# Performance work log

Hardware: AMD Instinct MI355X
Metric: run time of the kernel (lower is better)

Reference implementation:

```python
import jax, jax.numpy as jnp
import numpy as np

STATE = 256
IN = 128
OUT = 128


def setup_inputs() -> dict:
    key = jax.random.key(0)
    ks = jax.random.split(key, 10)
    u = jax.random.normal(ks[0], (8, 2048, IN), dtype=jnp.float32)
    x0_re = jax.random.normal(ks[1], (8, STATE), dtype=jnp.float32)
    x0_im = jax.random.normal(ks[2], (8, STATE), dtype=jnp.float32)
    # A init: 2*pi*rand angles on unit circle, scaled by 10 (enforce_stability=True)
    theta = 2.0 * jnp.pi * jax.random.uniform(ks[3], (STATE,), dtype=jnp.float32)
    A_re = 10.0 * jnp.cos(theta)
    A_im = 10.0 * jnp.sin(theta)
    # complex randn: real/imag parts each have variance 1/2
    inv_sqrt2 = 1.0 / np.sqrt(2.0)
    sB = inv_sqrt2 / np.sqrt(STATE + IN)
    B_re = jax.random.normal(ks[4], (IN, STATE), dtype=jnp.float32) * sB
    B_im = jax.random.normal(ks[5], (IN, STATE), dtype=jnp.float32) * sB
    sC = inv_sqrt2 / np.sqrt(STATE + OUT)
    C_re = jax.random.normal(ks[6], (STATE, OUT), dtype=jnp.float32) * sC
    C_im = jax.random.normal(ks[7], (STATE, OUT), dtype=jnp.float32) * sC
    D = jnp.zeros((IN, OUT), dtype=jnp.float32)
    b = jnp.zeros((OUT,), dtype=jnp.float32)
    return {"u": u, "x0_re": x0_re, "x0_im": x0_im, "A_re": A_re, "A_im": A_im,
            "B_re": B_re, "B_im": B_im, "C_re": C_re, "C_im": C_im, "D": D, "b": b}


def reference(u, x0_re, x0_im, A_re, A_im, B_re, B_im, C_re, C_im, D, b):
    cdt = jnp.complex64
    length = u.shape[1]
    A = (A_re + 1j * A_im).astype(cdt)
    # enforce_stability: map poles inside unit disc
    A = A / jnp.sqrt(A * jnp.conj(A) + 1.0)
    # Vandermonde powers A^t for t in [0, length]  -> [length+1, n]
    Aps = A[None, :] ** jnp.arange(length + 1)[:, None]
    Bm = (B_re + 1j * B_im).astype(cdt)
    uB = u.astype(cdt) @ Bm  # [batch, length, n]
    # FFT-based causal convolution of Aps[:-1] ([length, n]) with uB
    T = 2 ** int(np.ceil(np.log2(2 * length - 1)))
    AF = jnp.fft.fft(Aps[:-1], n=T, axis=0)      # [T, n]
    UF = jnp.fft.fft(uB, n=T, axis=1)            # [batch, T, n]
    x = jnp.fft.ifft(AF[None] * UF, axis=1)[:, :length]  # [batch, length, n]
    # add initial-state contribution A^t * x0
    x0 = (x0_re + 1j * x0_im).astype(cdt)
    x = x + Aps[1:][None] * x0[:, None, :]
    Cm = (C_re + 1j * C_im).astype(cdt)
    y = jnp.real(x @ Cm) + u @ D + b
    return y, x[:, -1]
```

## Files before the change

kernel.cpp:

```cpp
#include <hip/hip_runtime.h>
#include <math.h>

#define BATCH 8
#define T 2048
#define N 256
#define INF 128
#define OUTF 128
#define L 16
#define LOG2L 4
#define NC (T / L)
#define KTOT 640
#define NKS 20
#define NKU 4
#define UBS 516

typedef __attribute__((ext_vector_type(8))) short short8;
typedef __attribute__((ext_vector_type(4))) float f32x4;

__device__ __forceinline__ unsigned short f2b(float f) {
    union { float f; unsigned u; } x; x.f = f;
    unsigned r = (x.u + 0x7FFFu + ((x.u >> 16) & 1u)) >> 16;
    return (unsigned short)r;
}
__device__ __forceinline__ float b2f(unsigned short s) {
    union { unsigned u; float f; } x; x.u = ((unsigned)s) << 16;
    return x.f;
}

__global__ __launch_bounds__(256) void k_prep(const float* __restrict__ Are,
                                              const float* __restrict__ Aim,
                                              const float* __restrict__ Bre,
                                              const float* __restrict__ Bim,
                                              const float* __restrict__ Cre,
                                              const float* __restrict__ Cim,
                                              const float* __restrict__ D,
                                              float2* __restrict__ Apow,
                                              unsigned short* __restrict__ Bswz,
                                              unsigned short* __restrict__ Bswz2) {
    int blk = blockIdx.x;
    int tid = threadIdx.x;
    if (blk < 40) {
        int unit = blk * 4 + (tid >> 6);
        int ks = unit >> 3, ot = unit & 7;
        int l = tid & 63;
        int o = ot * 16 + (l & 15);
        int k0 = ks * 32 + (l >> 4) * 8;
        short8 out;
#pragma unroll
        for (int j = 0; j < 8; ++j) {
            int gk = k0 + j;
            float v = (gk < 256) ? Cre[gk * OUTF + o]
                    : (gk < 512) ? -Cim[(gk - 256) * OUTF + o]
                                 : D[(gk - 512) * OUTF + o];
            out[j] = (short)f2b(v);
        }
        *(short8*)(Bswz + ((size_t)unit * 64 + l) * 8) = out;
    } else if (blk < 72) {
        int unit = (blk - 40) * 4 + (tid >> 6);
        int l = tid & 63;
        int col = (unit & 31) * 16 + (l & 15);
        int k0 = (unit >> 5) * 32 + (l >> 4) * 8;
        short8 out;
#pragma unroll
        for (int j = 0; j < 8; ++j) {
            int gk = k0 + j;
            float v = (col < 256) ? Bre[gk * N + col] : Bim[gk * N + col - 256];
            out[j] = (short)f2b(v);
        }
        *(short8*)(Bswz2 + ((size_t)unit * 64 + l) * 8) = out;
    } else {
        int n = tid;
        float ar = Are[n], ai = Aim[n];
        float inv = 1.0f / sqrtf(ar * ar + ai * ai + 1.0f);
        ar *= inv; ai *= inv;
        float pr = ar, pi = ai;
        for (int j = 0; j < L; ++j) {
            Apow[j * N + n] = make_float2(pr, pi);
            float nr = pr * ar - pi * ai;
            float ni = pr * ai + pi * ar;
            pr = nr; pi = ni;
        }
    }
}

__global__ __launch_bounds__(512, 8) void kU_scan(const float* __restrict__ u,
                                                  const unsigned short* __restrict__ Bswz2,
                                                  const float2* __restrict__ Apow,
                                                  unsigned short* __restrict__ xbb,
                                                  float2* __restrict__ carr) {
    __shared__ float uB[16][UBS];
    int tid = threadIdx.x;
    int lane = tid & 63;
    int w = tid >> 6;
    size_t rowg0 = (size_t)blockIdx.x * 16;
    const float* uprow = u + (rowg0 + (lane & 15)) * INF + (lane >> 4) * 8;

    f32x4 acc[4];
#pragma unroll
    for (int i = 0; i < 4; ++i) acc[i] = (f32x4){0.f, 0.f, 0.f, 0.f};

    const short8* Bfr2 = (const short8*)Bswz2;
#pragma unroll
    for (int ks = 0; ks < NKU; ++ks) {
        float4 a0 = *(const float4*)(uprow + ks * 32);
        float4 a1 = *(const float4*)(uprow + ks * 32 + 4);
        short8 af;
        af[0] = (short)f2b(a0.x); af[1] = (short)f2b(a0.y);
        af[2] = (short)f2b(a0.z); af[3] = (short)f2b(a0.w);
        af[4] = (short)f2b(a1.x); af[5] = (short)f2b(a1.y);
        af[6] = (short)f2b(a1.z); af[7] = (short)f2b(a1.w);
#pragma unroll
        for (int i = 0; i < 4; ++i) {
            int ct = w * 4 + i;
            short8 bf = Bfr2[(size_t)(ks * 32 + ct) * 64 + lane];
            acc[i] = __builtin_amdgcn_mfma_f32_16x16x32_bf16(af, bf, acc[i], 0, 0, 0);
        }
    }
    {
        int rbase = (lane >> 4) * 4;
        int cb = lane & 15;
#pragma unroll
        for (int i = 0; i < 4; ++i) {
            int col = (w * 4 + i) * 16 + cb;
#pragma unroll
            for (int r = 0; r < 4; ++r)
                uB[rbase + r][col] = acc[i][r];
        }
    }
    __syncthreads();

    if (tid < 256) {
        int n = tid;
        int b = (int)(rowg0 >> 11);
        int c = (int)((rowg0 & 2047) >> LOG2L);
        float2 a = Apow[n];
        float xr = 0.f, xi = 0.f;
#pragma unroll
        for (int j = 0; j < 16; ++j) {
            float ur = uB[j][n];
            float ui = uB[j][256 + n];
            float nr = fmaf(a.x, xr, fmaf(-a.y, xi, ur));
            float ni = fmaf(a.x, xi, fmaf(a.y, xr, ui));
            xr = nr; xi = ni;
            size_t rowg = rowg0 + j;
            xbb[rowg * 512 + n]       = f2b(xr);
            xbb[rowg * 512 + 256 + n] = f2b(xi);
        }
        carr[((size_t)b * NC + c) * N + n] = make_float2(xr, xi);
    }
}

__global__ __launch_bounds__(256) void k2_carry(const float* __restrict__ x0re,
                                                const float* __restrict__ x0im,
                                                const float2* __restrict__ Apow,
                                                float2* __restrict__ carr,
                                                float* __restrict__ out_tail,
                                                int tail_mode) {
    int b = blockIdx.x, n = threadIdx.x;
    float pr = x0re[b * N + n], pi = x0im[b * N + n];
    float2 aL = Apow[(L - 1) * N + n];
#pragma unroll 8
    for (int c = 0; c < NC; ++c) {
        size_t off = ((size_t)b * NC + c) * N + n;
        float2 f = carr[off];
        carr[off] = make_float2(pr, pi);
        float nr = f.x + aL.x * pr - aL.y * pi;
        float ni = f.y + aL.x * pi + aL.y * pr;
        pr = nr; pi = ni;
    }
    if (tail_mode == 2) {
        out_tail[(b * N + n) * 2 + 0] = pr;
        out_tail[(b * N + n) * 2 + 1] = pi;
    } else if (tail_mode == 1) {
        out_tail[b * N + n] = pr;
    }
}

__global__ __launch_bounds__(256) void k3_mfma(const unsigned short* __restrict__ xbb,
                                               const float2* __restrict__ Apow,
                                               const float2* __restrict__ carr,
                                               const float* __restrict__ u,
                                               const unsigned short* __restrict__ Bswz,
                                               const float* __restrict__ bias,
                                               float* __restrict__ y) {
    __shared__ short8 Bs[2][1024];
    int tid = threadIdx.x;
    int lane = tid & 63;
    int w = tid >> 6;
    size_t rowg = (size_t)blockIdx.x * 64 + w * 16 + (lane & 15);
    int koff = (lane >> 4) * 8;
    int t = (int)(rowg & 2047);
    int b = (int)(rowg >> 11);
    int j = t & (L - 1);
    int c = t >> LOG2L;
    const float4* Ap4 = (const float4*)(Apow + (size_t)j * N);
    const float4* Cv4 = (const float4*)(carr + ((size_t)b * NC + c) * N);
    const unsigned short* arow = xbb + rowg * 512 + koff;
    const float* urow = u + rowg * INF + koff;
    const char* Bbytes = (const char*)Bswz;

    f32x4 acc[8];
#pragma unroll
    for (int ot = 0; ot < 8; ++ot) acc[ot] = (f32x4){0.f, 0.f, 0.f, 0.f};

    auto KApair = [](int p, int& ka, int& kb) {
        if (p < 8) { ka = p; kb = p + 8; }
        else if (p == 8) { ka = 16; kb = 17; }
        else { ka = 18; kb = 19; }
    };

    auto STAGEB = [&](int p, int buf) {
        int ka, kb; KApair(p, ka, kb);
#pragma unroll
        for (int i = 0; i < 4; ++i) {
            int seg = w * 4 + i;
            int k = (seg < 8) ? ka : kb;
            const char* src = Bbytes + (size_t)k * 8192 + (size_t)(seg & 7) * 1024 + (size_t)lane * 16;
            __builtin_amdgcn_global_load_lds(
                (const __attribute__((address_space(1))) unsigned int*)src,
                (__attribute__((address_space(3))) unsigned int*)((char*)&Bs[buf][0] + seg * 1024),
                16, 0, 0);
        }
    };

    STAGEB(0, 0);
    __syncthreads();

    int cur = 0;
    for (int p = 0; p < 10; ++p) {
        if (p < 9) STAGEB(p + 1, cur ^ 1);

        short8 afa, afb;
        if (p < 8) {
            short8 xre = *(const short8*)(arow + p * 32);
            short8 xim = *(const short8*)(arow + (p + 8) * 32);
            int n0 = p * 32 + koff;
            float4 ap[4], vv[4];
#pragma unroll
            for (int q = 0; q < 4; ++q) {
                ap[q] = Ap4[(n0 >> 1) + q];
                vv[q] = Cv4[(n0 >> 1) + q];
            }
#pragma unroll
            for (int e = 0; e < 8; ++e) {
                float4 aq = ap[e >> 1];
                float4 vq = vv[e >> 1];
                float pr = (e & 1) ? aq.z : aq.x;
                float pi = (e & 1) ? aq.w : aq.y;
                float vr = (e & 1) ? vq.z : vq.x;
                float vi = (e & 1) ? vq.w : vq.y;
                afa[e] = (short)f2b(b2f((unsigned short)xre[e]) + (pr * vr - pi * vi));
                afb[e] = (short)f2b(b2f((unsigned short)xim[e]) + (pr * vi + pi * vr));
            }
        } else {
            int ks2a = (p == 8) ? 0 : 2;
            float4 a0 = *(const float4*)(urow + ks2a * 32);
            float4 a1 = *(const float4*)(urow + ks2a * 32 + 4);
            afa[0] = (short)f2b(a0.x); afa[1] = (short)f2b(a0.y);
            afa[2] = (short)f2b(a0.z); afa[3] = (short)f2b(a0.w);
            afa[4] = (short)f2b(a1.x); afa[5] = (short)f2b(a1.y);
            afa[6] = (short)f2b(a1.z); afa[7] = (short)f2b(a1.w);
            float4 b0 = *(const float4*)(urow + (ks2a + 1) * 32);
            float4 b1 = *(const float4*)(urow + (ks2a + 1) * 32 + 4);
            afb[0] = (short)f2b(b0.x); afb[1] = (short)f2b(b0.y);
            afb[2] = (short)f2b(b0.z); afb[3] = (short)f2b(b0.w);
            afb[4] = (short)f2b(b1.x); afb[5] = (short)f2b(b1.y);
            afb[6] = (short)f2b(b1.z); afb[7] = (short)f2b(b1.w);
        }

#pragma unroll
        for (int ot = 0; ot < 8; ++ot) {
            short8 bf = Bs[cur][ot * 64 + lane];
            acc[ot] = __builtin_amdgcn_mfma_f32_16x16x32_bf16(afa, bf, acc[ot], 0, 0, 0);
        }
#pragma unroll
        for (int ot = 0; ot < 8; ++ot) {
            short8 bf = Bs[cur][512 + ot * 64 + lane];
            acc[ot] = __builtin_amdgcn_mfma_f32_16x16x32_bf16(afb, bf, acc[ot], 0, 0, 0);
        }

        __syncthreads();
        cur ^= 1;
    }

    int colb = lane & 15;
    int rq = lane >> 4;
    size_t rowout = (size_t)blockIdx.x * 64 + w * 16 + rq * 4;
#pragma unroll
    for (int ot = 0; ot < 8; ++ot) {
        int o = ot * 16 + colb;
        float bv = bias[o];
#pragma unroll
        for (int r = 0; r < 4; ++r) {
            y[(rowout + r) * OUTF + o] = acc[ot][r] + bv;
        }
    }
}

extern "C" void kernel_launch(void* const* d_in, const int* in_sizes, int n_in,
                              void* d_out, int out_size, void* d_ws, size_t ws_size,
                              hipStream_t stream) {
    const float* u    = (const float*)d_in[0];
    const float* x0re = (const float*)d_in[1];
    const float* x0im = (const float*)d_in[2];
    const float* Are  = (const float*)d_in[3];
    const float* Aim  = (const float*)d_in[4];
    const float* Bre  = (const float*)d_in[5];
    const float* Bim  = (const float*)d_in[6];
    const float* Cre  = (const float*)d_in[7];
    const float* Cim  = (const float*)d_in[8];
    const float* D    = (const float*)d_in[9];
    const float* bias = (const float*)d_in[10];
    float* y = (float*)d_out;

    char* ws = (char*)d_ws;
    float2* Apow = (float2*)ws;
    char* p = ws + (size_t)L * N * sizeof(float2);
    float2* carr = (float2*)p;
    p += (size_t)BATCH * NC * N * sizeof(float2);
    unsigned short* xbb = (unsigned short*)p;
    p += (size_t)BATCH * T * 512 * sizeof(unsigned short);
    unsigned short* Bswz = (unsigned short*)p;
    p += (size_t)NKS * 8 * 64 * 8 * sizeof(unsigned short);
    unsigned short* Bswz2 = (unsigned short*)p;

    const int ysz = BATCH * T * OUTF;
    const int tail_elems = out_size - ysz;
    int tail_mode = (tail_elems >= BATCH * N * 2) ? 2
                  : (tail_elems >= BATCH * N) ? 1 : 0;
    float* tail = y + ysz;

    k_prep<<<73, 256, 0, stream>>>(Are, Aim, Bre, Bim, Cre, Cim, D, Apow, Bswz, Bswz2);
    kU_scan<<<BATCH * NC, 512, 0, stream>>>(u, Bswz2, Apow, xbb, carr);
    k2_carry<<<BATCH, 256, 0, stream>>>(x0re, x0im, Apow, carr, tail, tail_mode);
    k3_mfma<<<(BATCH * T) / 64, 256, 0, stream>>>(xbb, Apow, carr, u, Bswz, bias, y);
}
```

Before: 55.12 us.

## Stage scan output through LDS for vectorized stores and prefetch A operands

In the chunk-scan kernel, per-step scattered 2-byte bf16 stores of the state are replaced by writing the fp32 state back into the shared uB tile, then a cooperative pass packs rows into 16-byte bf16 vector stores. In the output GEMM kernel, the x/Apow/Cv and u fragment loads for the next k-step are issued before the current MFMAs, a software prefetch that hides global load latency. This costs an extra barrier and LDS round trip, and more live registers.

Result: no change. 54.49 us (median of 3 runs) (-1.1%).

```diff
diff --git a/kernel.cpp b/kernel.cpp
--- a/kernel.cpp
+++ b/kernel.cpp
@@ -142,11 +142,29 @@
             float nr = fmaf(a.x, xr, fmaf(-a.y, xi, ur));
             float ni = fmaf(a.x, xi, fmaf(a.y, xr, ui));
             xr = nr; xi = ni;
-            size_t rowg = rowg0 + j;
-            xbb[rowg * 512 + n]       = f2b(xr);
-            xbb[rowg * 512 + 256 + n] = f2b(xi);
+            uB[j][n] = xr;
+            uB[j][256 + n] = xi;
         }
         carr[((size_t)b * NC + c) * N + n] = make_float2(xr, xi);
+    }
+    __syncthreads();
+
+    {
+        int row = tid & 15;
+        int cg  = tid >> 4;
+#pragma unroll
+        for (int half = 0; half < 2; ++half) {
+            int col0 = half * 256 + cg * 8;
+            const float4* s4 = (const float4*)&uB[row][col0];
+            float4 v0 = s4[0];
+            float4 v1 = s4[1];
+            short8 st;
+            st[0] = (short)f2b(v0.x); st[1] = (short)f2b(v0.y);
+            st[2] = (short)f2b(v0.z); st[3] = (short)f2b(v0.w);
+            st[4] = (short)f2b(v1.x); st[5] = (short)f2b(v1.y);
+            st[6] = (short)f2b(v1.z); st[7] = (short)f2b(v1.w);
+            *(short8*)(xbb + (rowg0 + row) * 512 + col0) = st;
+        }
     }
 }
 
@@ -223,7 +241,27 @@
         }
     };
 
+    short8 xre, xim;
+    float4 ap0, ap1, ap2, ap3, vv0, vv1, vv2, vv3;
+    float4 ua0, ua1, ub0, ub1;
+
+    auto LOADX = [&](int p) {
+        xre = *(const short8*)(arow + p * 32);
+        xim = *(const short8*)(arow + (p + 8) * 32);
+        int f4 = (p * 32 + koff) >> 1;
+        ap0 = Ap4[f4];     ap1 = Ap4[f4 + 1]; ap2 = Ap4[f4 + 2]; ap3 = Ap4[f4 + 3];
+        vv0 = Cv4[f4];     vv1 = Cv4[f4 + 1]; vv2 = Cv4[f4 + 2]; vv3 = Cv4[f4 + 3];
+    };
+    auto LOADU = [&](int p) {
+        int k = (p == 8) ? 0 : 2;
+        ua0 = *(const float4*)(urow + k * 32);
+        ua1 = *(const float4*)(urow + k * 32 + 4);
+        ub0 = *(const float4*)(urow + (k + 1) * 32);
+        ub1 = *(const float4*)(urow + (k + 1) * 32 + 4);
+    };
+
     STAGEB(0, 0);
+    LOADX(0);
     __syncthreads();
 
     int cur = 0;
@@ -232,15 +270,8 @@
 
         short8 afa, afb;
         if (p < 8) {
-            short8 xre = *(const short8*)(arow + p * 32);
-            short8 xim = *(const short8*)(arow + (p + 8) * 32);
-            int n0 = p * 32 + koff;
-            float4 ap[4], vv[4];
-#pragma unroll
-            for (int q = 0; q < 4; ++q) {
-                ap[q] = Ap4[(n0 >> 1) + q];
-                vv[q] = Cv4[(n0 >> 1) + q];
-            }
+            float4 ap[4] = {ap0, ap1, ap2, ap3};
+            float4 vv[4] = {vv0, vv1, vv2, vv3};
 #pragma unroll
             for (int e = 0; e < 8; ++e) {
                 float4 aq = ap[e >> 1];
@@ -253,20 +284,18 @@
                 afb[e] = (short)f2b(b2f((unsigned short)xim[e]) + (pr * vi + pi * vr));
             }
         } else {
-            int ks2a = (p == 8) ? 0 : 2;
-            float4 a0 = *(const float4*)(urow + ks2a * 32);
-            float4 a1 = *(const float4*)(urow + ks2a * 32 + 4);
-            afa[0] = (short)f2b(a0.x); afa[1] = (short)f2b(a0.y);
-            afa[2] = (short)f2b(a0.z); afa[3] = (short)f2b(a0.w);
-            afa[4] = (short)f2b(a1.x); afa[5] = (short)f2b(a1.y);
-            afa[6] = (short)f2b(a1.z); afa[7] = (short)f2b(a1.w);
-            float4 b0 = *(const float4*)(urow + (ks2a + 1) * 32);
-            float4 b1 = *(const float4*)(urow + (ks2a + 1) * 32 + 4);
-            afb[0] = (short)f2b(b0.x); afb[1] = (short)f2b(b0.y);
-            afb[2] = (short)f2b(b0.z); afb[3] = (short)f2b(b0.w);
-            afb[4] = (short)f2b(b1.x); afb[5] = (short)f2b(b1.y);
-            afb[6] = (short)f2b(b1.z); afb[7] = (short)f2b(b1.w);
-        }
+            afa[0] = (short)f2b(ua0.x); afa[1] = (short)f2b(ua0.y);
+            afa[2] = (short)f2b(ua0.z); afa[3] = (short)f2b(ua0.w);
+            afa[4] = (short)f2b(ua1.x); afa[5] = (short)f2b(ua1.y);
+            afa[6] = (short)f2b(ua1.z); afa[7] = (short)f2b(ua1.w);
+            afb[0] = (short)f2b(ub0.x); afb[1] = (short)f2b(ub0.y);
+            afb[2] = (short)f2b(ub0.z); afb[3] = (short)f2b(ub0.w);
+            afb[4] = (short)f2b(ub1.x); afb[5] = (short)f2b(ub1.y);
+            afb[6] = (short)f2b(ub1.z); afb[7] = (short)f2b(ub1.w);
+        }
+
+        if (p < 7)      LOADX(p + 1);
+        else if (p < 9) LOADU(p + 1);
 
 #pragma unroll
         for (int ot = 0; ot < 8; ++ot) {
```
